# Performance work log

Measured on AMD Instinct MI355X. Metric: run time of the kernel, lower is better.

Reference implementation:

```python
import jax, jax.numpy as jnp
import numpy as np

D_IN = 256
D_OUT = 256

def setup_inputs() -> dict:
    key = jax.random.key(0)
    kx, kq, kk, kv = jax.random.split(key, 4)
    x = jax.random.normal(kx, (8, D_IN, 64, 64), dtype=jnp.float32)
    s = 1.0 / np.sqrt(D_IN)
    Wq = jax.random.normal(kq, (D_OUT, D_IN), dtype=jnp.float32) * s
    Wk = jax.random.normal(kk, (D_OUT, D_IN), dtype=jnp.float32) * s
    Wv = jax.random.normal(kv, (D_OUT, D_IN), dtype=jnp.float32) * s
    return {"x": x, "Wq": Wq, "Wk": Wk, "Wv": Wv}

def reference(x, Wq, Wk, Wv):
    b, c_in, h, w = x.shape
    c = Wq.shape[0]
    # 1x1 conv == channel linear; tokens along N = h*w
    xt = x.reshape(b, c_in, h * w).transpose(0, 2, 1)      # (b, N, c_in)
    q = jnp.einsum('bnc,dc->bnd', xt, Wq)                  # (b, N, c)
    k = jnp.einsum('bnc,dc->bnd', xt, Wk)
    v = jnp.einsum('bnc,dc->bnd', xt, Wv)
    wei = jnp.einsum('bnd,bmd->bnm', q, k) / jnp.sqrt(jnp.asarray(c, x.dtype))
    wei = jax.nn.softmax(wei, axis=-1)
    out = jnp.einsum('bnm,bmd->bnd', wei, v)               # (b, N, c)
    return out.transpose(0, 2, 1).reshape(b, c, h, w)
```

## Files before the change

### kernel.cpp

```cpp
#include <hip/hip_runtime.h>

#define DIN 256
#define NTOK 4096

typedef __bf16 bf16;
typedef __bf16 bf16x4 __attribute__((ext_vector_type(4)));
typedef __bf16 bf16x8 __attribute__((ext_vector_type(8)));
typedef float floatx16 __attribute__((ext_vector_type(16)));

__device__ inline floatx16 mfma32(bf16x8 a, bf16x8 b, floatx16 c) {
    return __builtin_amdgcn_mfma_f32_32x32x16_bf16(a, b, c, 0, 0, 0);
}

__device__ inline void async16(const void* g, void* l) {
    __builtin_amdgcn_global_load_lds(
        (const __attribute__((address_space(1))) unsigned int*)g,
        (__attribute__((address_space(3))) unsigned int*)l, 16, 0, 0);
}

__global__ void convert_w(const float* __restrict__ wq, const float* __restrict__ wk,
                          const float* __restrict__ wv, bf16* __restrict__ Wb) {
    int i = blockIdx.x * 256 + threadIdx.x;
    const float* src = (i < 65536) ? wq : (i < 131072 ? wk : wv);
    Wb[i] = (bf16)src[i & 65535];
}

__global__ __launch_bounds__(512, 2) void proj_kernel(
    const float* __restrict__ x, const bf16* __restrict__ Wb,
    bf16* __restrict__ Qo, bf16* __restrict__ Ko, bf16* __restrict__ Vo)
{
    __shared__ __attribute__((aligned(16))) char smem[131072];
    bf16 (*xs)[264] = (bf16(*)[264])smem;
    bf16* bufA = (bf16*)smem;
    bf16* bufB = (bf16*)(smem + 65536);

    int bid = blockIdx.x;
    int b = bid & 7, nt = bid >> 3;
    int n0 = nt * 128;
    int t = threadIdx.x;
    int lane = t & 63, w = t >> 6;
    int l32 = lane & 31, h = lane >> 5;
    int tokg = w >> 1;
    int og   = w & 1;

    int wofs[8];
#pragma unroll
    for (int jj = 0; jj < 8; ++jj) {
        int q = w * 8 + jj;
        int r2 = 2 * q + h;
        int cs = l32 ^ (r2 & 31);
        wofs[jj] = r2 * 512 + cs * 16;
    }

    {
        const float* xb = x + (size_t)b * DIN * NTOK;
#pragma unroll
        for (int it = 0; it < 16; ++it) {
            int flat = it * 512 + t;
            int c = flat >> 5;
            int nf = flat & 31;
            float4 v = *(const float4*)(xb + (size_t)c * NTOK + n0 + nf * 4);
            int nn = nf * 4;
            xs[nn + 0][c] = (bf16)v.x;
            xs[nn + 1][c] = (bf16)v.y;
            xs[nn + 2][c] = (bf16)v.z;
            xs[nn + 3][c] = (bf16)v.w;
        }
    }
    __syncthreads();

    bf16x8 xf[16];
#pragma unroll
    for (int ks = 0; ks < 16; ++ks)
        xf[ks] = *(const bf16x8*)&xs[tokg * 32 + l32][ks * 16 + h * 8];

    __syncthreads();

    {
        const char* src = (const char*)Wb;
#pragma unroll
        for (int jj = 0; jj < 8; ++jj)
            async16(src + wofs[jj], (char*)bufA + (w * 8 + jj) * 1024);
    }
    __syncthreads();

    for (int p = 0; p < 6; ++p) {
        if (p < 5) {
            bf16* nb = ((p + 1) & 1) ? bufB : bufA;
            const char* src = (const char*)Wb + (size_t)(p + 1) * 65536;
#pragma unroll
            for (int jj = 0; jj < 8; ++jj)
                async16(src + wofs[jj], (char*)nb + (w * 8 + jj) * 1024);
        }

        const bf16* wb = (p & 1) ? bufB : bufA;
        int mat = p >> 1, dhalf = p & 1;

        floatx16 acc[2];
#pragma unroll
        for (int dc = 0; dc < 2; ++dc)
#pragma unroll
            for (int i = 0; i < 16; ++i) acc[dc][i] = 0.0f;

        if (mat < 2) {
#pragma unroll
            for (int ks = 0; ks < 16; ++ks) {
#pragma unroll
                for (int dc = 0; dc < 2; ++dc) {
                    int row = og * 64 + dc * 32 + l32;
                    bf16x8 wf = *(const bf16x8*)((const char*)wb + row * 512 +
                                                 (((2 * ks + h) ^ (row & 31)) * 16));
                    acc[dc] = mfma32(xf[ks], wf, acc[dc]);
                }
            }
            bf16* Out = (mat == 0 ? Qo : Ko) + (size_t)b * NTOK * DIN;
#pragma unroll
            for (int dc = 0; dc < 2; ++dc) {
                int d = dhalf * 128 + og * 64 + dc * 32 + l32;
#pragma unroll
                for (int r = 0; r < 16; ++r) {
                    int tok = n0 + tokg * 32 + (r & 3) + 8 * (r >> 2) + 4 * h;
                    Out[(size_t)tok * DIN + d] = (bf16)acc[dc][r];
                }
            }
        } else {
#pragma unroll
            for (int ks = 0; ks < 16; ++ks) {
#pragma unroll
                for (int dc = 0; dc < 2; ++dc) {
                    int row = og * 64 + dc * 32 + l32;
                    bf16x8 wf = *(const bf16x8*)((const char*)wb + row * 512 +
                                                 (((2 * ks + h) ^ (row & 31)) * 16));
                    acc[dc] = mfma32(wf, xf[ks], acc[dc]);
                }
            }
            bf16* Out = Vo + (size_t)b * DIN * NTOK;
            int tok = n0 + tokg * 32 + l32;
#pragma unroll
            for (int dc = 0; dc < 2; ++dc)
#pragma unroll
                for (int r = 0; r < 16; ++r) {
                    int d = dhalf * 128 + og * 64 + dc * 32 + (r & 3) + 8 * (r >> 2) + 4 * h;
                    Out[(size_t)d * NTOK + tok] = (bf16)acc[dc][r];
                }
        }
        __syncthreads();
    }
}

__global__ __launch_bounds__(512, 2) void attn_kernel(
    const bf16* __restrict__ Q, const bf16* __restrict__ K,
    const bf16* __restrict__ V, float* __restrict__ out)
{
    __shared__ bf16 Ks[2][64][256];
    __shared__ bf16 Vs[2][256][64];
    __shared__ bf16 Ps[2][128][64];

    int bid = blockIdx.x;
    int b = bid & 7, qt = bid >> 3;
    int n0 = qt * 128;
    int t = threadIdx.x, lane = t & 63, w = t >> 6;
    int l32 = lane & 31, h = lane >> 5;
    int lkey = (l32 & 7) ^ ((l32 >> 3) & 3);

    const bf16* Qb = Q + (size_t)b * NTOK * DIN;
    const bf16* Kb = K + (size_t)b * NTOK * DIN;
    const bf16* Vb = V + (size_t)b * DIN * NTOK;
    float* Lp = (float*)&Ps[0][0][0];

    if (w < 4) {
        int tokg = w >> 1, mg = w & 1;
        int krow = mg * 32 + l32;

        int koff[8];
#pragma unroll
        for (int jj = 0; jj < 8; ++jj) {
            int q = w * 8 + jj;
            int r = q * 2 + (lane >> 5);
            int ck = (lane & 31) ^ ((r & 7) ^ ((r >> 3) & 3));
            koff[jj] = (r * 256 + ck * 8) * 2;
        }

        bf16x8 qf[2][16];
#pragma unroll
        for (int ca = 0; ca < 2; ++ca) {
            const bf16* qrow = Qb + (size_t)(n0 + tokg * 64 + ca * 32 + l32) * DIN + h * 8;
#pragma unroll
            for (int ks = 0; ks < 16; ++ks) qf[ca][ks] = *(const bf16x8*)(qrow + ks * 16);
        }

        float lsum[2] = {0.0f, 0.0f};

#pragma unroll
        for (int jj = 0; jj < 8; ++jj) {
            async16((const char*)Kb + koff[jj], (bf16*)Ks[0] + (w * 8 + jj) * 512);
            async16((const char*)Kb + 32768 + koff[jj], (bf16*)Ks[1] + (w * 8 + jj) * 512);
        }
        __syncthreads();

        {
            const bf16* Krd = (const bf16*)Ks[0] + krow * 256;
            floatx16 st[2];
#pragma unroll
            for (int i = 0; i < 16; ++i) { st[0][i] = 0.0f; st[1][i] = 0.0f; }
#pragma unroll
            for (int ks = 0; ks < 16; ++ks) {
                bf16x8 kf = *(const bf16x8*)(Krd + (((2 * ks + h) ^ lkey) * 8));
                st[0] = mfma32(kf, qf[0][ks], st[0]);
                st[1] = mfma32(kf, qf[1][ks], st[1]);
            }
#pragma unroll
            for (int ca = 0; ca < 2; ++ca) {
                bf16* Prow = (bf16*)Ps[0] + (tokg * 64 + ca * 32 + l32) * 64;
                float tsum = 0.0f;
#pragma unroll
                for (int g = 0; g < 4; ++g) {
                    bf16x4 pk;
#pragma unroll
                    for (int i = 0; i < 4; ++i) {
                        float e = __expf(st[ca][g * 4 + i] * 0.0625f);
                        tsum += e;
                        pk[i] = (bf16)e;
                    }
                    *(bf16x4*)((char*)Prow + (((mg * 4 + g) ^ lkey) * 16) + h * 8) = pk;
                }
                lsum[ca] += tsum;
            }
        }
        __syncthreads();

        for (int mt = 0; mt < 64; ++mt) {
            if (mt < 62) {
                int kadd = (mt + 2) * 32768;
#pragma unroll
                for (int jj = 0; jj < 8; ++jj)
                    async16((const char*)Kb + kadd + koff[jj],
                            (bf16*)Ks[mt & 1] + (w * 8 + jj) * 512);
            }
            if (mt < 63) {
                const bf16* Krd = (const bf16*)Ks[(mt + 1) & 1] + krow * 256;
                floatx16 st[2];
#pragma unroll
                for (int i = 0; i < 16; ++i) { st[0][i] = 0.0f; st[1][i] = 0.0f; }
#pragma unroll
                for (int ks = 0; ks < 16; ++ks) {
                    bf16x8 kf = *(const bf16x8*)(Krd + (((2 * ks + h) ^ lkey) * 8));
                    st[0] = mfma32(kf, qf[0][ks], st[0]);
                    st[1] = mfma32(kf, qf[1][ks], st[1]);
                }
                bf16* Pw = (bf16*)Ps[(mt + 1) & 1];
#pragma unroll
                for (int ca = 0; ca < 2; ++ca) {
                    bf16* Prow = Pw + (tokg * 64 + ca * 32 + l32) * 64;
                    float tsum = 0.0f;
#pragma unroll
                    for (int g = 0; g < 4; ++g) {
                        bf16x4 pk;
#pragma unroll
                        for (int i = 0; i < 4; ++i) {
                            float e = __expf(st[ca][g * 4 + i] * 0.0625f);
                            tsum += e;
                            pk[i] = (bf16)e;
                        }
                        *(bf16x4*)((char*)Prow + (((mg * 4 + g) ^ lkey) * 16) + h * 8) = pk;
                    }
                    lsum[ca] += tsum;
                }
            }
            __syncthreads();
        }

#pragma unroll
        for (int ca = 0; ca < 2; ++ca) {
            float sv = lsum[ca];
            sv += __shfl_xor(sv, 32);
            if (h == 0) Lp[mg * 128 + tokg * 64 + ca * 32 + l32] = sv;
        }
        __syncthreads();
    } else {
        int slab = w - 4;

        int vofs[8];
#pragma unroll
        for (int jj = 0; jj < 8; ++jj) {
            int q = slab * 8 + jj;
            int d = q * 8 + (lane >> 3);
            int cv = (lane & 7) ^ ((d & 7) ^ ((d >> 3) & 3));
            vofs[jj] = (d * 4096 + cv * 8) * 2;
        }

        floatx16 oacc[8];
#pragma unroll
        for (int i = 0; i < 8; ++i)
            for (int j = 0; j < 16; ++j) oacc[i][j] = 0.0f;

#pragma unroll
        for (int jj = 0; jj < 8; ++jj)
            async16((const char*)Vb + vofs[jj], (bf16*)Vs[0] + (slab * 8 + jj) * 512);
        __syncthreads();
        __syncthreads();

        for (int mt = 0; mt < 64; ++mt) {
            if (mt < 63) {
                int vadd = (mt + 1) * 128;
#pragma unroll
                for (int jj = 0; jj < 8; ++jj)
                    async16((const char*)Vb + vadd + vofs[jj],
                            (bf16*)Vs[(mt + 1) & 1] + (slab * 8 + jj) * 512);
            }
            const bf16* Vrd = (const bf16*)Vs[mt & 1];
            const char* Prd = (const char*)Ps[mt & 1];
#pragma unroll
            for (int kst = 0; kst < 4; ++kst) {
                bf16x8 va[2], pb[4];
#pragma unroll
                for (int dc = 0; dc < 2; ++dc) {
                    int d = slab * 64 + dc * 32 + l32;
                    va[dc] = *(const bf16x8*)(Vrd + d * 64 + (((kst * 2 + h) ^ lkey) * 8));
                }
#pragma unroll
                for (int tc = 0; tc < 4; ++tc)
                    pb[tc] = *(const bf16x8*)(Prd + (tc * 32 + l32) * 128 +
                                              (((kst * 2 + h) ^ lkey) * 16));
#pragma unroll
                for (int dc = 0; dc < 2; ++dc)
#pragma unroll
                    for (int tc = 0; tc < 4; ++tc)
                        oacc[dc * 4 + tc] = mfma32(va[dc], pb[tc], oacc[dc * 4 + tc]);
            }
            __syncthreads();
        }

        __syncthreads();
        float* ob = out + (size_t)b * DIN * NTOK;
#pragma unroll
        for (int tc = 0; tc < 4; ++tc) {
            int tok = tc * 32 + l32;
            float rinv = 1.0f / (Lp[tok] + Lp[128 + tok]);
#pragma unroll
            for (int dc = 0; dc < 2; ++dc)
#pragma unroll
                for (int r = 0; r < 16; ++r) {
                    int d = slab * 64 + dc * 32 + (r & 3) + 8 * (r >> 2) + 4 * h;
                    ob[(size_t)d * NTOK + n0 + tok] = oacc[dc * 4 + tc][r] * rinv;
                }
        }
    }
}

extern "C" void kernel_launch(void* const* d_in, const int* in_sizes, int n_in,
                              void* d_out, int out_size, void* d_ws, size_t ws_size,
                              hipStream_t stream) {
    const float* x  = (const float*)d_in[0];
    const float* wq = (const float*)d_in[1];
    const float* wk = (const float*)d_in[2];
    const float* wv = (const float*)d_in[3];
    float* outf = (float*)d_out;

    char* ws = (char*)d_ws;
    bf16* Wb = (bf16*)(ws);
    bf16* Qp = (bf16*)(ws + (1u << 20));
    bf16* Kp = (bf16*)(ws + (1u << 20) + (16u << 20));
    bf16* Vp = (bf16*)(ws + (1u << 20) + (32u << 20));

    convert_w<<<768, 256, 0, stream>>>(wq, wk, wv, Wb);
    proj_kernel<<<256, 512, 0, stream>>>(x, Wb, Qp, Kp, Vp);
    attn_kernel<<<256, 512, 0, stream>>>(Qp, Kp, Vp, outf);
}
```

Baseline: 237.4 us.

## Triple-buffer K in LDS and load V directly into registers

K tiles move to a three-stage LDS ring buffer with explicit vmcnt waits and raw s_barrier, so the producer waves keep two tiles in flight instead of one. The consumer waves stop staging V through LDS. They double-buffer V fragments in registers straight from global memory, and only P still goes through LDS. This removes the V LDS traffic and the full __syncthreads waits that drained all loads. In exchange it adds VGPR pressure and relies on hand-tuned waitcnt counts being correct.

```diff
diff --git a/kernel.cpp b/kernel.cpp
--- a/kernel.cpp
+++ b/kernel.cpp
@@ -152,8 +152,7 @@
     const bf16* __restrict__ Q, const bf16* __restrict__ K,
     const bf16* __restrict__ V, float* __restrict__ out)
 {
-    __shared__ bf16 Ks[2][64][256];
-    __shared__ bf16 Vs[2][256][64];
+    __shared__ bf16 Ks[3][64][256];
     __shared__ bf16 Ps[2][128][64];
 
     int bid = blockIdx.x;
@@ -192,11 +191,20 @@
         float lsum[2] = {0.0f, 0.0f};
 
 #pragma unroll
-        for (int jj = 0; jj < 8; ++jj) {
+        for (int jj = 0; jj < 8; ++jj)
             async16((const char*)Kb + koff[jj], (bf16*)Ks[0] + (w * 8 + jj) * 512);
+#pragma unroll
+        for (int jj = 0; jj < 8; ++jj)
             async16((const char*)Kb + 32768 + koff[jj], (bf16*)Ks[1] + (w * 8 + jj) * 512);
-        }
-        __syncthreads();
+#pragma unroll
+        for (int jj = 0; jj < 8; ++jj)
+            async16((const char*)Kb + 65536 + koff[jj], (bf16*)Ks[2] + (w * 8 + jj) * 512);
+
+        __builtin_amdgcn_sched_barrier(0);
+        asm volatile("s_waitcnt vmcnt(16)" ::: "memory");
+        __builtin_amdgcn_sched_barrier(0);
+        __builtin_amdgcn_s_barrier();
+        __builtin_amdgcn_sched_barrier(0);
 
         {
             const bf16* Krd = (const bf16*)Ks[0] + krow * 256;
@@ -227,28 +235,34 @@
                 lsum[ca] += tsum;
             }
         }
-        __syncthreads();
-
-        for (int mt = 0; mt < 64; ++mt) {
-            if (mt < 62) {
-                int kadd = (mt + 2) * 32768;
+        __builtin_amdgcn_sched_barrier(0);
+        asm volatile("s_waitcnt vmcnt(8) lgkmcnt(0)" ::: "memory");
+        __builtin_amdgcn_sched_barrier(0);
+        __builtin_amdgcn_s_barrier();
+        __builtin_amdgcn_sched_barrier(0);
+
+        int br = 1, bd = 0;
+#pragma unroll 1
+        for (int i = 0; i < 64; ++i) {
+            if (i < 61) {
+                int kadd = (i + 3) * 32768;
 #pragma unroll
                 for (int jj = 0; jj < 8; ++jj)
                     async16((const char*)Kb + kadd + koff[jj],
-                            (bf16*)Ks[mt & 1] + (w * 8 + jj) * 512);
-            }
-            if (mt < 63) {
-                const bf16* Krd = (const bf16*)Ks[(mt + 1) & 1] + krow * 256;
+                            (bf16*)Ks[bd] + (w * 8 + jj) * 512);
+            }
+            if (i < 63) {
+                const bf16* Krd = (const bf16*)Ks[br] + krow * 256;
                 floatx16 st[2];
 #pragma unroll
-                for (int i = 0; i < 16; ++i) { st[0][i] = 0.0f; st[1][i] = 0.0f; }
+                for (int ii = 0; ii < 16; ++ii) { st[0][ii] = 0.0f; st[1][ii] = 0.0f; }
 #pragma unroll
                 for (int ks = 0; ks < 16; ++ks) {
                     bf16x8 kf = *(const bf16x8*)(Krd + (((2 * ks + h) ^ lkey) * 8));
                     st[0] = mfma32(kf, qf[0][ks], st[0]);
                     st[1] = mfma32(kf, qf[1][ks], st[1]);
                 }
-                bf16* Pw = (bf16*)Ps[(mt + 1) & 1];
+                bf16* Pw = (bf16*)Ps[(i + 1) & 1];
 #pragma unroll
                 for (int ca = 0; ca < 2; ++ca) {
                     bf16* Prow = Pw + (tokg * 64 + ca * 32 + l32) * 64;
@@ -257,17 +271,22 @@
                     for (int g = 0; g < 4; ++g) {
                         bf16x4 pk;
 #pragma unroll
-                        for (int i = 0; i < 4; ++i) {
-                            float e = __expf(st[ca][g * 4 + i] * 0.0625f);
+                        for (int ii = 0; ii < 4; ++ii) {
+                            float e = __expf(st[ca][g * 4 + ii] * 0.0625f);
                             tsum += e;
-                            pk[i] = (bf16)e;
+                            pk[ii] = (bf16)e;
                         }
                         *(bf16x4*)((char*)Prow + (((mg * 4 + g) ^ lkey) * 16) + h * 8) = pk;
                     }
                     lsum[ca] += tsum;
                 }
             }
-            __syncthreads();
+            __builtin_amdgcn_sched_barrier(0);
+            asm volatile("s_waitcnt vmcnt(8) lgkmcnt(0)" ::: "memory");
+            __builtin_amdgcn_sched_barrier(0);
+            __builtin_amdgcn_s_barrier();
+            __builtin_amdgcn_sched_barrier(0);
+            bd = br; br = (br == 2) ? 0 : br + 1;
         }
 
 #pragma unroll
@@ -280,55 +299,84 @@
     } else {
         int slab = w - 4;
 
-        int vofs[8];
-#pragma unroll
-        for (int jj = 0; jj < 8; ++jj) {
-            int q = slab * 8 + jj;
-            int d = q * 8 + (lane >> 3);
-            int cv = (lane & 7) ^ ((d & 7) ^ ((d >> 3) & 3));
-            vofs[jj] = (d * 4096 + cv * 8) * 2;
-        }
+        const bf16* Vr0 = Vb + (size_t)(slab * 64 + l32) * NTOK + h * 8;
+        const bf16* Vr1 = Vb + (size_t)(slab * 64 + 32 + l32) * NTOK + h * 8;
 
         floatx16 oacc[8];
 #pragma unroll
         for (int i = 0; i < 8; ++i)
             for (int j = 0; j < 16; ++j) oacc[i][j] = 0.0f;
 
-#pragma unroll
-        for (int jj = 0; jj < 8; ++jj)
-            async16((const char*)Vb + vofs[jj], (bf16*)Vs[0] + (slab * 8 + jj) * 512);
-        __syncthreads();
-        __syncthreads();
-
-        for (int mt = 0; mt < 64; ++mt) {
-            if (mt < 63) {
-                int vadd = (mt + 1) * 128;
-#pragma unroll
-                for (int jj = 0; jj < 8; ++jj)
-                    async16((const char*)Vb + vadd + vofs[jj],
-                            (bf16*)Vs[(mt + 1) & 1] + (slab * 8 + jj) * 512);
-            }
-            const bf16* Vrd = (const bf16*)Vs[mt & 1];
-            const char* Prd = (const char*)Ps[mt & 1];
-#pragma unroll
-            for (int kst = 0; kst < 4; ++kst) {
-                bf16x8 va[2], pb[4];
-#pragma unroll
-                for (int dc = 0; dc < 2; ++dc) {
-                    int d = slab * 64 + dc * 32 + l32;
-                    va[dc] = *(const bf16x8*)(Vrd + d * 64 + (((kst * 2 + h) ^ lkey) * 8));
-                }
-#pragma unroll
-                for (int tc = 0; tc < 4; ++tc)
-                    pb[tc] = *(const bf16x8*)(Prd + (tc * 32 + l32) * 128 +
-                                              (((kst * 2 + h) ^ lkey) * 16));
-#pragma unroll
-                for (int dc = 0; dc < 2; ++dc)
+        bf16x8 vaA[8], vaB[8];
+#pragma unroll
+        for (int kst = 0; kst < 4; ++kst) {
+            vaA[kst]     = *(const bf16x8*)(Vr0 + kst * 16);
+            vaA[4 + kst] = *(const bf16x8*)(Vr1 + kst * 16);
+        }
+        __builtin_amdgcn_s_barrier();
+        __builtin_amdgcn_sched_barrier(0);
+        __builtin_amdgcn_s_barrier();
+        __builtin_amdgcn_sched_barrier(0);
+
+#pragma unroll 1
+        for (int j = 0; j < 32; ++j) {
+            int i = 2 * j;
+            {
+                int nn = (i + 1) * 64;
+#pragma unroll
+                for (int kst = 0; kst < 4; ++kst) {
+                    vaB[kst]     = *(const bf16x8*)(Vr0 + nn + kst * 16);
+                    vaB[4 + kst] = *(const bf16x8*)(Vr1 + nn + kst * 16);
+                }
+                const char* Prd = (const char*)Ps[0];
+#pragma unroll
+                for (int kst = 0; kst < 4; ++kst) {
+                    bf16x8 pb[4];
 #pragma unroll
                     for (int tc = 0; tc < 4; ++tc)
-                        oacc[dc * 4 + tc] = mfma32(va[dc], pb[tc], oacc[dc * 4 + tc]);
-            }
-            __syncthreads();
+                        pb[tc] = *(const bf16x8*)(Prd + (tc * 32 + l32) * 128 +
+                                                  (((kst * 2 + h) ^ lkey) * 16));
+#pragma unroll
+                    for (int tc = 0; tc < 4; ++tc) {
+                        oacc[tc]     = mfma32(vaA[kst],     pb[tc], oacc[tc]);
+                        oacc[4 + tc] = mfma32(vaA[4 + kst], pb[tc], oacc[4 + tc]);
+                    }
+                }
+                __builtin_amdgcn_sched_barrier(0);
+                asm volatile("s_waitcnt lgkmcnt(0)" ::: "memory");
+                __builtin_amdgcn_sched_barrier(0);
+                __builtin_amdgcn_s_barrier();
+                __builtin_amdgcn_sched_barrier(0);
+            }
+            {
+                if (j < 31) {
+                    int nn = (i + 2) * 64;
+#pragma unroll
+                    for (int kst = 0; kst < 4; ++kst) {
+                        vaA[kst]     = *(const bf16x8*)(Vr0 + nn + kst * 16);
+                        vaA[4 + kst] = *(const bf16x8*)(Vr1 + nn + kst * 16);
+                    }
+                }
+                const char* Prd = (const char*)Ps[1];
+#pragma unroll
+                for (int kst = 0; kst < 4; ++kst) {
+                    bf16x8 pb[4];
+#pragma unroll
+                    for (int tc = 0; tc < 4; ++tc)
+                        pb[tc] = *(const bf16x8*)(Prd + (tc * 32 + l32) * 128 +
+                                                  (((kst * 2 + h) ^ lkey) * 16));
+#pragma unroll
+                    for (int tc = 0; tc < 4; ++tc) {
+                        oacc[tc]     = mfma32(vaB[kst],     pb[tc], oacc[tc]);
+                        oacc[4 + tc] = mfma32(vaB[4 + kst], pb[tc], oacc[4 + tc]);
+                    }
+                }
+                __builtin_amdgcn_sched_barrier(0);
+                asm volatile("s_waitcnt lgkmcnt(0)" ::: "memory");
+                __builtin_amdgcn_sched_barrier(0);
+                __builtin_amdgcn_s_barrier();
+                __builtin_amdgcn_sched_barrier(0);
+            }
         }
 
         __syncthreads();
```

After: 238.0 us. About the same (+0.3%).

## Rebalance attention warp roles: 4 QK waves, 8 PV waves at 768 threads

Applied to the files above, without the earlier changes.

Raises the attention block from 512 to 768 threads. Each of the 4 score waves now owns 32 query rows against all 64 keys instead of 64 rows against 32 keys. The PV work is split across 8 waves, each holding 4 accumulators instead of 8, so the row-sum needs no cross-wave combine and PV MFMA throughput per block rises. Lower register pressure per PV wave and more waves per block aim to balance the producer and consumer stages. The catch is that launch_bounds(768,3) tightens the register budget and may cause spills or lower occupancy given the large LDS footprint.

```diff
diff --git a/kernel.cpp b/kernel.cpp
--- a/kernel.cpp
+++ b/kernel.cpp
@@ -148,7 +148,7 @@
     }
 }
 
-__global__ __launch_bounds__(512, 2) void attn_kernel(
+__global__ __launch_bounds__(768, 3) void attn_kernel(
     const bf16* __restrict__ Q, const bf16* __restrict__ K,
     const bf16* __restrict__ V, float* __restrict__ out)
 {
@@ -169,27 +169,25 @@
     float* Lp = (float*)&Ps[0][0][0];
 
     if (w < 4) {
-        int tokg = w >> 1, mg = w & 1;
-        int krow = mg * 32 + l32;
+        int qg = w;
 
         int koff[8];
 #pragma unroll
         for (int jj = 0; jj < 8; ++jj) {
             int q = w * 8 + jj;
-            int r = q * 2 + (lane >> 5);
-            int ck = (lane & 31) ^ ((r & 7) ^ ((r >> 3) & 3));
+            int r = q * 2 + h;
+            int ck = l32 ^ ((r & 7) ^ ((r >> 3) & 3));
             koff[jj] = (r * 256 + ck * 8) * 2;
         }
 
-        bf16x8 qf[2][16];
-#pragma unroll
-        for (int ca = 0; ca < 2; ++ca) {
-            const bf16* qrow = Qb + (size_t)(n0 + tokg * 64 + ca * 32 + l32) * DIN + h * 8;
-#pragma unroll
-            for (int ks = 0; ks < 16; ++ks) qf[ca][ks] = *(const bf16x8*)(qrow + ks * 16);
-        }
-
-        float lsum[2] = {0.0f, 0.0f};
+        bf16x8 qf[16];
+        {
+            const bf16* qrow = Qb + (size_t)(n0 + qg * 32 + l32) * DIN + h * 8;
+#pragma unroll
+            for (int ks = 0; ks < 16; ++ks) qf[ks] = *(const bf16x8*)(qrow + ks * 16);
+        }
+
+        float lsum = 0.0f;
 
 #pragma unroll
         for (int jj = 0; jj < 8; ++jj) {
@@ -199,36 +197,38 @@
         __syncthreads();
 
         {
-            const bf16* Krd = (const bf16*)Ks[0] + krow * 256;
-            floatx16 st[2];
-#pragma unroll
-            for (int i = 0; i < 16; ++i) { st[0][i] = 0.0f; st[1][i] = 0.0f; }
+            const bf16* Krd = (const bf16*)Ks[0] + l32 * 256;
+            floatx16 st0, st1;
+#pragma unroll
+            for (int i = 0; i < 16; ++i) { st0[i] = 0.0f; st1[i] = 0.0f; }
 #pragma unroll
             for (int ks = 0; ks < 16; ++ks) {
-                bf16x8 kf = *(const bf16x8*)(Krd + (((2 * ks + h) ^ lkey) * 8));
-                st[0] = mfma32(kf, qf[0][ks], st[0]);
-                st[1] = mfma32(kf, qf[1][ks], st[1]);
-            }
-#pragma unroll
-            for (int ca = 0; ca < 2; ++ca) {
-                bf16* Prow = (bf16*)Ps[0] + (tokg * 64 + ca * 32 + l32) * 64;
-                float tsum = 0.0f;
+                int co = ((2 * ks + h) ^ lkey) * 8;
+                bf16x8 kf0 = *(const bf16x8*)(Krd + co);
+                bf16x8 kf1 = *(const bf16x8*)(Krd + 32 * 256 + co);
+                st0 = mfma32(kf0, qf[ks], st0);
+                st1 = mfma32(kf1, qf[ks], st1);
+            }
+            bf16* Prow = (bf16*)Ps[0] + (qg * 32 + l32) * 64;
+#pragma unroll
+            for (int kvb = 0; kvb < 2; ++kvb) {
 #pragma unroll
                 for (int g = 0; g < 4; ++g) {
                     bf16x4 pk;
 #pragma unroll
                     for (int i = 0; i < 4; ++i) {
-                        float e = __expf(st[ca][g * 4 + i] * 0.0625f);
-                        tsum += e;
+                        float sval = kvb ? st1[g * 4 + i] : st0[g * 4 + i];
+                        float e = __expf(sval * 0.0625f);
+                        lsum += e;
                         pk[i] = (bf16)e;
                     }
-                    *(bf16x4*)((char*)Prow + (((mg * 4 + g) ^ lkey) * 16) + h * 8) = pk;
-                }
-                lsum[ca] += tsum;
-            }
-        }
-        __syncthreads();
-
+                    *(bf16x4*)((char*)Prow + (((kvb * 4 + g) ^ lkey) * 16) + h * 8) = pk;
+                }
+            }
+        }
+        __syncthreads();
+
+#pragma unroll 1
         for (int mt = 0; mt < 64; ++mt) {
             if (mt < 62) {
                 int kadd = (mt + 2) * 32768;
@@ -238,95 +238,92 @@
                             (bf16*)Ks[mt & 1] + (w * 8 + jj) * 512);
             }
             if (mt < 63) {
-                const bf16* Krd = (const bf16*)Ks[(mt + 1) & 1] + krow * 256;
-                floatx16 st[2];
-#pragma unroll
-                for (int i = 0; i < 16; ++i) { st[0][i] = 0.0f; st[1][i] = 0.0f; }
+                const bf16* Krd = (const bf16*)Ks[(mt + 1) & 1] + l32 * 256;
+                floatx16 st0, st1;
+#pragma unroll
+                for (int i = 0; i < 16; ++i) { st0[i] = 0.0f; st1[i] = 0.0f; }
 #pragma unroll
                 for (int ks = 0; ks < 16; ++ks) {
-                    bf16x8 kf = *(const bf16x8*)(Krd + (((2 * ks + h) ^ lkey) * 8));
-                    st[0] = mfma32(kf, qf[0][ks], st[0]);
-                    st[1] = mfma32(kf, qf[1][ks], st[1]);
-                }
-                bf16* Pw = (bf16*)Ps[(mt + 1) & 1];
-#pragma unroll
-                for (int ca = 0; ca < 2; ++ca) {
-                    bf16* Prow = Pw + (tokg * 64 + ca * 32 + l32) * 64;
-                    float tsum = 0.0f;
+                    int co = ((2 * ks + h) ^ lkey) * 8;
+                    bf16x8 kf0 = *(const bf16x8*)(Krd + co);
+                    bf16x8 kf1 = *(const bf16x8*)(Krd + 32 * 256 + co);
+                    st0 = mfma32(kf0, qf[ks], st0);
+                    st1 = mfma32(kf1, qf[ks], st1);
+                }
+                bf16* Prow = (bf16*)Ps[(mt + 1) & 1] + (qg * 32 + l32) * 64;
+#pragma unroll
+                for (int kvb = 0; kvb < 2; ++kvb) {
 #pragma unroll
                     for (int g = 0; g < 4; ++g) {
                         bf16x4 pk;
 #pragma unroll
                         for (int i = 0; i < 4; ++i) {
-                            float e = __expf(st[ca][g * 4 + i] * 0.0625f);
-                            tsum += e;
+                            float sval = kvb ? st1[g * 4 + i] : st0[g * 4 + i];
+                            float e = __expf(sval * 0.0625f);
+                            lsum += e;
                             pk[i] = (bf16)e;
                         }
-                        *(bf16x4*)((char*)Prow + (((mg * 4 + g) ^ lkey) * 16) + h * 8) = pk;
+                        *(bf16x4*)((char*)Prow + (((kvb * 4 + g) ^ lkey) * 16) + h * 8) = pk;
                     }
-                    lsum[ca] += tsum;
                 }
             }
             __syncthreads();
         }
 
-#pragma unroll
-        for (int ca = 0; ca < 2; ++ca) {
-            float sv = lsum[ca];
+        {
+            float sv = lsum;
             sv += __shfl_xor(sv, 32);
-            if (h == 0) Lp[mg * 128 + tokg * 64 + ca * 32 + l32] = sv;
+            if (h == 0) Lp[qg * 32 + l32] = sv;
         }
         __syncthreads();
     } else {
-        int slab = w - 4;
-
-        int vofs[8];
-#pragma unroll
-        for (int jj = 0; jj < 8; ++jj) {
-            int q = slab * 8 + jj;
+        int ws = w - 4;
+        int slab2 = ws >> 1;
+        int qh = ws & 1;
+
+        int vofs[4];
+#pragma unroll
+        for (int jj = 0; jj < 4; ++jj) {
+            int q = ws * 4 + jj;
             int d = q * 8 + (lane >> 3);
             int cv = (lane & 7) ^ ((d & 7) ^ ((d >> 3) & 3));
             vofs[jj] = (d * 4096 + cv * 8) * 2;
         }
 
-        floatx16 oacc[8];
-#pragma unroll
-        for (int i = 0; i < 8; ++i)
+        floatx16 oacc[4];
+#pragma unroll
+        for (int i = 0; i < 4; ++i)
             for (int j = 0; j < 16; ++j) oacc[i][j] = 0.0f;
 
 #pragma unroll
-        for (int jj = 0; jj < 8; ++jj)
-            async16((const char*)Vb + vofs[jj], (bf16*)Vs[0] + (slab * 8 + jj) * 512);
-        __syncthreads();
-        __syncthreads();
-
+        for (int jj = 0; jj < 4; ++jj)
+            async16((const char*)Vb + vofs[jj], (bf16*)Vs[0] + (ws * 4 + jj) * 512);
+        __syncthreads();
+        __syncthreads();
+
+#pragma unroll 1
         for (int mt = 0; mt < 64; ++mt) {
             if (mt < 63) {
                 int vadd = (mt + 1) * 128;
 #pragma unroll
-                for (int jj = 0; jj < 8; ++jj)
+                for (int jj = 0; jj < 4; ++jj)
                     async16((const char*)Vb + vadd + vofs[jj],
-                            (bf16*)Vs[(mt + 1) & 1] + (slab * 8 + jj) * 512);
+                            (bf16*)Vs[(mt + 1) & 1] + (ws * 4 + jj) * 512);
             }
             const bf16* Vrd = (const bf16*)Vs[mt & 1];
             const char* Prd = (const char*)Ps[mt & 1];
 #pragma unroll
             for (int kst = 0; kst < 4; ++kst) {
-                bf16x8 va[2], pb[4];
-#pragma unroll
-                for (int dc = 0; dc < 2; ++dc) {
-                    int d = slab * 64 + dc * 32 + l32;
-                    va[dc] = *(const bf16x8*)(Vrd + d * 64 + (((kst * 2 + h) ^ lkey) * 8));
-                }
-#pragma unroll
-                for (int tc = 0; tc < 4; ++tc)
-                    pb[tc] = *(const bf16x8*)(Prd + (tc * 32 + l32) * 128 +
-                                              (((kst * 2 + h) ^ lkey) * 16));
-#pragma unroll
-                for (int dc = 0; dc < 2; ++dc)
-#pragma unroll
-                    for (int tc = 0; tc < 4; ++tc)
-                        oacc[dc * 4 + tc] = mfma32(va[dc], pb[tc], oacc[dc * 4 + tc]);
+                int co = ((kst * 2 + h) ^ lkey);
+                int d0 = slab2 * 64 + l32;
+                bf16x8 va0 = *(const bf16x8*)(Vrd + d0 * 64 + co * 8);
+                bf16x8 va1 = *(const bf16x8*)(Vrd + (d0 + 32) * 64 + co * 8);
+                bf16x8 pb0 = *(const bf16x8*)(Prd + (qh * 64 + l32) * 128 + co * 16);
+                bf16x8 pb1 = *(const bf16x8*)(Prd + (qh * 64 + 32 + l32) * 128 + co * 16);
+                oacc[0] = mfma32(va0, pb0, oacc[0]);
+                oacc[1] = mfma32(va0, pb1, oacc[1]);
+                oacc[2] = mfma32(va1, pb0, oacc[2]);
+                oacc[3] = mfma32(va1, pb1, oacc[3]);
             }
             __syncthreads();
         }
@@ -334,15 +331,15 @@
         __syncthreads();
         float* ob = out + (size_t)b * DIN * NTOK;
 #pragma unroll
-        for (int tc = 0; tc < 4; ++tc) {
-            int tok = tc * 32 + l32;
-            float rinv = 1.0f / (Lp[tok] + Lp[128 + tok]);
+        for (int tc = 0; tc < 2; ++tc) {
+            int tokl = qh * 64 + tc * 32 + l32;
+            float rinv = 1.0f / Lp[tokl];
 #pragma unroll
             for (int dc = 0; dc < 2; ++dc)
 #pragma unroll
                 for (int r = 0; r < 16; ++r) {
-                    int d = slab * 64 + dc * 32 + (r & 3) + 8 * (r >> 2) + 4 * h;
-                    ob[(size_t)d * NTOK + n0 + tok] = oacc[dc * 4 + tc][r] * rinv;
+                    int d = slab2 * 64 + dc * 32 + (r & 3) + 8 * (r >> 2) + 4 * h;
+                    ob[(size_t)d * NTOK + n0 + tokl] = oacc[dc * 2 + tc][r] * rinv;
                 }
         }
     }
@@ -365,5 +362,5 @@
 
     convert_w<<<768, 256, 0, stream>>>(wq, wk, wv, Wb);
     proj_kernel<<<256, 512, 0, stream>>>(x, Wb, Qp, Kp, Vp);
-    attn_kernel<<<256, 512, 0, stream>>>(Qp, Kp, Vp, outf);
-}
+    attn_kernel<<<256, 768, 0, stream>>>(Qp, Kp, Vp, outf);
+}
```

After: 244.9 us. 3.2% more time.
